# Kernel tuning notes

Hardware: AMD Instinct MI355X
Metric: run time of the kernel (lower is better)

Reference implementation:

```python
import jax, jax.numpy as jnp
import numpy as np

F6_E3M2_MAX = 28.0  # max representable e3m2 value
M_TOKENS, K_IN, N_OUT = 256, 4096, 4096


def _quantize_e3m2(w: np.ndarray) -> np.ndarray:
    """Round-to-nearest onto the FP6 e3m2 grid (bias=3, min normal 2^-2, subnormal step 2^-4)."""
    sign = np.sign(w)
    a = np.minimum(np.abs(w), F6_E3M2_MAX)
    e = np.clip(np.floor(np.log2(np.maximum(a, 1e-30))), -2.0, 4.0)
    step = np.exp2(e - 2.0)  # 2 mantissa bits -> 4 steps per octave; subnormal step = 2^-4
    q = np.round(a / step) * step
    return (sign * np.minimum(q, F6_E3M2_MAX)).astype(np.float32)


def setup_inputs() -> dict:
    key = jax.random.key(0)
    k_x, k_w, k_b = jax.random.split(key, 3)
    x = (jax.random.normal(k_x, (M_TOKENS, K_IN), dtype=jnp.float32)).astype(jnp.float16)
    w_fp32 = np.asarray(jax.random.normal(k_w, (N_OUT, K_IN), dtype=jnp.float32)) * 0.02
    # per-row scale as in to_scaled_tc_float6_e3m2
    amax = np.clip(np.abs(w_fp32).max(axis=1), 1e-12, None)
    scale = F6_E3M2_MAX / amax                       # quantization scale
    weight_fp6 = _quantize_e3m2(w_fp32 * scale[:, None])  # values on the e3m2 grid
    scales = jnp.asarray(1.0 / scale, dtype=jnp.float16)  # dequant scale (stored half)
    bias = (jax.random.normal(k_b, (N_OUT,), dtype=jnp.float32) * 0.01).astype(jnp.float16)
    return {
        "x": x,
        "weight_fp6": jnp.asarray(weight_fp6),
        "scales": scales,
        "bias": bias,
    }


def reference(x, weight_fp6, scales, bias):
    # Fused dequant + GEMM: W = weight_fp6 * row_scale; out = x @ W^T + bias
    in_features = weight_fp6.shape[1]
    x2d = x.reshape(-1, in_features).astype(jnp.float16)
    w_deq = weight_fp6 * scales.astype(jnp.float32)[:, None]  # [N, K] fp32
    out = jnp.einsum("mk,nk->mn", x2d.astype(jnp.float32), w_deq,
                     preferred_element_type=jnp.float32)       # fp32 accumulate (split-K sums in fp32)
    out = out.astype(jnp.float16) + bias
    return out.reshape(*x.shape[:-1], weight_fp6.shape[0]).astype(x.dtype)
```

## Files before the change

kernel.cpp:

```cpp
#include <hip/hip_runtime.h>
#include <hip/hip_fp16.h>


typedef __attribute__((ext_vector_type(8))) _Float16 half8;
typedef __attribute__((ext_vector_type(2))) __fp16 fp16x2;
typedef __attribute__((ext_vector_type(4))) float f32x4;

typedef const __attribute__((address_space(1))) void* gptr_t;
typedef __attribute__((address_space(3))) void* lptr_t;

constexpr int K = 4096, N = 4096, M = 256;
constexpr int BM = 128, BN = 128, BK = 32;
constexpr int SPL = 8;
constexpr int KSPL = K / SPL;
constexpr int NT = KSPL / BK;

__device__ __forceinline__ void gload16(const void* g, void* l) {
    __builtin_amdgcn_global_load_lds((gptr_t)g, (lptr_t)l, 16, 0, 0);
}

__device__ __forceinline__ half8 cvt8(float4 f0, float4 f1) {
    fp16x2 p0 = __builtin_amdgcn_cvt_pkrtz(f0.x, f0.y);
    fp16x2 p1 = __builtin_amdgcn_cvt_pkrtz(f0.z, f0.w);
    fp16x2 p2 = __builtin_amdgcn_cvt_pkrtz(f1.x, f1.y);
    fp16x2 p3 = __builtin_amdgcn_cvt_pkrtz(f1.z, f1.w);
    half8 h;
    h[0]=(_Float16)p0[0]; h[1]=(_Float16)p0[1];
    h[2]=(_Float16)p1[0]; h[3]=(_Float16)p1[1];
    h[4]=(_Float16)p2[0]; h[5]=(_Float16)p2[1];
    h[6]=(_Float16)p3[0]; h[7]=(_Float16)p3[1];
    return h;
}

__global__ __launch_bounds__(256)
void xcvt(const float* __restrict__ X, _Float16* __restrict__ X16)
{
    const int i = ((int)blockIdx.x * 256 + (int)threadIdx.x) * 8;
    float4 a = *(const float4*)(X + i);
    float4 b = *(const float4*)(X + i + 4);
    *(half8*)(X16 + i) = cvt8(a, b);
}

__global__ __launch_bounds__(256, 3)
void gemm(const _Float16* __restrict__ X16,
          const float* __restrict__ W,
          float* __restrict__ P)
{
    __shared__ __align__(16) _Float16 LA[2][BM * BK];
    __shared__ __align__(16) float    LB[2][BN * BK];

    const int tid = (int)threadIdx.x;
    const int l   = tid & 63;
    const int wv  = tid >> 6;
    const int lc  = l & 15;
    const int lr  = l >> 4;
    const int wm  = (wv & 1) * 64;
    const int wn  = (wv >> 1) * 64;

    const int bid = (int)blockIdx.x;
    const int xcd = bid & 7;
    const int i   = bid >> 3;
    const int mb  = i & 1;
    const int sp  = (i >> 1) & 7;
    const int nbl = i >> 4;
    const int bm  = mb * BM;
    const int bn  = (xcd * 4 + nbl) * BN;
    const int kb  = sp * KSPL;

    const int arow = wv * 32 + (l >> 2);
    const int acho = ((l & 3) ^ ((l >> 3) & 3)) * 8;
    const _Float16* ag0 = X16 + (size_t)(bm + arow)      * K + kb + acho;
    const _Float16* ag1 = X16 + (size_t)(bm + arow + 16) * K + kb + acho;
    const int asl0 = (wv * 32) * BK;
    const int asl1 = (wv * 32 + 16) * BK;
    const int wrow = wv * 32 + (l >> 3);
    const int wcho = ((l & 7) ^ (l >> 3)) * 4;
    const float* wg0 = W + (size_t)(bn + wrow)      * K + kb + wcho;
    const float* wg1 = W + (size_t)(bn + wrow + 8)  * K + kb + wcho;
    const float* wg2 = W + (size_t)(bn + wrow + 16) * K + kb + wcho;
    const float* wg3 = W + (size_t)(bn + wrow + 24) * K + kb + wcho;
    const int wsl0 = (wv * 32 + 0)  * BK;
    const int wsl1 = (wv * 32 + 8)  * BK;
    const int wsl2 = (wv * 32 + 16) * BK;
    const int wsl3 = (wv * 32 + 24) * BK;

#define STAGE(t, bf) do {                                               \
        gload16(ag0 + (size_t)(t) * BK, &LA[bf][asl0]);                 \
        gload16(ag1 + (size_t)(t) * BK, &LA[bf][asl1]);                 \
        gload16(wg0 + (size_t)(t) * BK, &LB[bf][wsl0]);                 \
        gload16(wg1 + (size_t)(t) * BK, &LB[bf][wsl1]);                 \
        gload16(wg2 + (size_t)(t) * BK, &LB[bf][wsl2]);                 \
        gload16(wg3 + (size_t)(t) * BK, &LB[bf][wsl3]);                 \
    } while (0)

    const int aswz = (lr ^ ((lc >> 1) & 3)) << 3;
    const int wsz0 = (((lr << 1))     ^ (lc & 7)) << 2;
    const int wsz1 = (((lr << 1) | 1) ^ (lc & 7)) << 2;

    f32x4 acc[4][4];
    #pragma unroll
    for (int a = 0; a < 4; ++a)
        #pragma unroll
        for (int b = 0; b < 4; ++b)
            acc[a][b] = (f32x4){0.f, 0.f, 0.f, 0.f};

#define COMPUTE(bf) do {                                                \
        half8 af[4];                                                    \
        _Pragma("unroll")                                               \
        for (int ar = 0; ar < 4; ++ar)                                  \
            af[ar] = *(const half8*)(&LA[bf][(wm + ar * 16 + lc) * BK + aswz]); \
        _Pragma("unroll")                                               \
        for (int br = 0; br < 4; ++br) {                                \
            const float* pw = &LB[bf][(wn + br * 16 + lc) * BK];        \
            float4 b0 = *(const float4*)(pw + wsz0);                    \
            float4 b1 = *(const float4*)(pw + wsz1);                    \
            half8 bb = cvt8(b0, b1);                                    \
            acc[0][br] = __builtin_amdgcn_mfma_f32_16x16x32_f16(af[0], bb, acc[0][br], 0, 0, 0); \
            acc[1][br] = __builtin_amdgcn_mfma_f32_16x16x32_f16(af[1], bb, acc[1][br], 0, 0, 0); \
            acc[2][br] = __builtin_amdgcn_mfma_f32_16x16x32_f16(af[2], bb, acc[2][br], 0, 0, 0); \
            acc[3][br] = __builtin_amdgcn_mfma_f32_16x16x32_f16(af[3], bb, acc[3][br], 0, 0, 0); \
        } } while (0)

    STAGE(0, 0);

    for (int t = 0; t < NT; ++t) {
        if (t + 1 < NT) {
            STAGE(t + 1, (t + 1) & 1);
            asm volatile("s_waitcnt vmcnt(6)" ::: "memory");
        } else {
            asm volatile("s_waitcnt vmcnt(0)" ::: "memory");
        }
        __builtin_amdgcn_sched_barrier(0);
        __builtin_amdgcn_s_barrier();
        __builtin_amdgcn_sched_barrier(0);
        COMPUTE(t & 1);
        __builtin_amdgcn_sched_barrier(0);
        __builtin_amdgcn_s_barrier();
    }
#undef STAGE
#undef COMPUTE

    float* Pb = P + (size_t)sp * M * N;
    const int orow = bm + wm + lr * 4;
    const int ocol = bn + wn + lc;
    #pragma unroll
    for (int ar = 0; ar < 4; ++ar)
        #pragma unroll
        for (int br = 0; br < 4; ++br)
            #pragma unroll
            for (int r = 0; r < 4; ++r)
                Pb[(size_t)(orow + ar * 16 + r) * N + ocol + br * 16] = acc[ar][br][r];
}

template <int SPLT>
__global__ __launch_bounds__(256)
void finalize(const float* __restrict__ P,
              const float* __restrict__ S,
              const float* __restrict__ Bi,
              float* __restrict__ O)
{
    const size_t i = ((size_t)blockIdx.x * 256 + threadIdx.x) * 4;
    const int n = (int)(i & (N - 1));
    float4 v = *(const float4*)(P + i);
    #pragma unroll
    for (int s = 1; s < SPLT; ++s) {
        float4 u = *(const float4*)(P + (size_t)s * M * N + i);
        v.x += u.x; v.y += u.y; v.z += u.z; v.w += u.w;
    }
    float4 sc = *(const float4*)(S + n);
    float4 bb = *(const float4*)(Bi + n);
    v.x = (float)(_Float16)((float)(_Float16)(v.x * sc.x) + bb.x);
    v.y = (float)(_Float16)((float)(_Float16)(v.y * sc.y) + bb.y);
    v.z = (float)(_Float16)((float)(_Float16)(v.z * sc.z) + bb.z);
    v.w = (float)(_Float16)((float)(_Float16)(v.w * sc.w) + bb.w);
    *(float4*)(O + i) = v;
}

__global__ __launch_bounds__(256)
void fp6lin_small(const float* __restrict__ X, const float* __restrict__ W,
                  const float* __restrict__ S, const float* __restrict__ Bi,
                  float* __restrict__ O)
{
    const int n = (int)blockIdx.x;
    const int m = (int)threadIdx.x;
    float s = 0.f;
    for (int k = 0; k < K; ++k)
        s += (float)(_Float16)X[(size_t)m * K + k] * (float)(_Float16)W[(size_t)n * K + k];
    O[(size_t)m * N + n] = (float)(_Float16)((float)(_Float16)(s * S[n]) + Bi[n]);
}

extern "C" void kernel_launch(void* const* d_in, const int* in_sizes, int n_in,
                              void* d_out, int out_size, void* d_ws, size_t ws_size,
                              hipStream_t stream) {
    const float* x  = (const float*)d_in[0];
    const float* w  = (const float*)d_in[1];
    const float* s  = (const float*)d_in[2];
    const float* bi = (const float*)d_in[3];
    float* o = (float*)d_out;

    const size_t xbytes = (size_t)M * K * 2;
    const size_t slice  = (size_t)M * N * sizeof(float);
    _Float16* x16 = (_Float16*)d_ws;
    float*    P   = (float*)((char*)d_ws + xbytes);
    const int fin_grid = M * N / 4 / 256;

    if (ws_size >= xbytes + SPL * slice) {
        xcvt<<<dim3(M * K / 8 / 256), dim3(256), 0, stream>>>(x, x16);
        gemm<<<dim3(2 * 4 * SPL * 8), dim3(256), 0, stream>>>(x16, w, P);
        finalize<SPL><<<dim3(fin_grid), dim3(256), 0, stream>>>(P, s, bi, o);
    } else {
        fp6lin_small<<<dim3(N), dim3(M), 0, stream>>>(x, w, s, bi, o);
    }
}
```

Measured before the change: 36.75 us.

## Fuse convert, GEMM and split-K reduce into one cooperative kernel

Merges the x fp32-to-fp16 conversion, the split-K GEMM and the finalize reduction into a single cooperative kernel, with grid-wide syncs between the phases. This removes two kernel launches and their inter-kernel gaps. In exchange it adds two grid barriers, and the fused kernel must keep 512 blocks co-resident. If the cooperative launch fails, it falls back to the three separate kernels.

```diff
diff --git a/kernel.cpp b/kernel.cpp
--- a/kernel.cpp
+++ b/kernel.cpp
@@ -1,5 +1,8 @@
 #include <hip/hip_runtime.h>
 #include <hip/hip_fp16.h>
+#include <hip/hip_cooperative_groups.h>
+
+namespace cg = cooperative_groups;
 
 
 typedef __attribute__((ext_vector_type(8))) _Float16 half8;
@@ -32,19 +35,9 @@
     return h;
 }
 
-__global__ __launch_bounds__(256)
-void xcvt(const float* __restrict__ X, _Float16* __restrict__ X16)
-{
-    const int i = ((int)blockIdx.x * 256 + (int)threadIdx.x) * 8;
-    float4 a = *(const float4*)(X + i);
-    float4 b = *(const float4*)(X + i + 4);
-    *(half8*)(X16 + i) = cvt8(a, b);
-}
-
-__global__ __launch_bounds__(256, 3)
-void gemm(const _Float16* __restrict__ X16,
-          const float* __restrict__ W,
-          float* __restrict__ P)
+__device__ __forceinline__ void gemm_body(const _Float16* __restrict__ X16,
+                                          const float* __restrict__ W,
+                                          float* __restrict__ P)
 {
     __shared__ __align__(16) _Float16 LA[2][BM * BK];
     __shared__ __align__(16) float    LB[2][BN * BK];
@@ -122,7 +115,6 @@
         } } while (0)
 
     STAGE(0, 0);
-
     for (int t = 0; t < NT; ++t) {
         if (t + 1 < NT) {
             STAGE(t + 1, (t + 1) & 1);
@@ -152,18 +144,69 @@
                 Pb[(size_t)(orow + ar * 16 + r) * N + ocol + br * 16] = acc[ar][br][r];
 }
 
-template <int SPLT>
+__global__ __launch_bounds__(256, 3)
+void fused(const float* __restrict__ X, const float* __restrict__ W,
+           const float* __restrict__ S, const float* __restrict__ Bi,
+           float* __restrict__ O, _Float16* __restrict__ X16,
+           float* __restrict__ P)
+{
+    {
+        const int i = ((int)blockIdx.x * 256 + (int)threadIdx.x) * 8;
+        float4 a = *(const float4*)(X + i);
+        float4 b = *(const float4*)(X + i + 4);
+        *(half8*)(X16 + i) = cvt8(a, b);
+    }
+    cg::this_grid().sync();
+    gemm_body(X16, W, P);
+    cg::this_grid().sync();
+    {
+        const int gt = (int)blockIdx.x * 256 + (int)threadIdx.x;
+        #pragma unroll
+        for (int rep = 0; rep < 2; ++rep) {
+            const size_t i = ((size_t)(gt * 2 + rep)) * 4;
+            const int n = (int)(i & (N - 1));
+            float4 v = *(const float4*)(P + i);
+            #pragma unroll
+            for (int s = 1; s < SPL; ++s) {
+                float4 u = *(const float4*)(P + (size_t)s * M * N + i);
+                v.x += u.x; v.y += u.y; v.z += u.z; v.w += u.w;
+            }
+            float4 sc = *(const float4*)(S + n);
+            float4 bb = *(const float4*)(Bi + n);
+            v.x = (float)(_Float16)((float)(_Float16)(v.x * sc.x) + bb.x);
+            v.y = (float)(_Float16)((float)(_Float16)(v.y * sc.y) + bb.y);
+            v.z = (float)(_Float16)((float)(_Float16)(v.z * sc.z) + bb.z);
+            v.w = (float)(_Float16)((float)(_Float16)(v.w * sc.w) + bb.w);
+            *(float4*)(O + i) = v;
+        }
+    }
+}
+
 __global__ __launch_bounds__(256)
-void finalize(const float* __restrict__ P,
-              const float* __restrict__ S,
-              const float* __restrict__ Bi,
-              float* __restrict__ O)
+void xcvt(const float* __restrict__ X, _Float16* __restrict__ X16)
+{
+    const int i = ((int)blockIdx.x * 256 + (int)threadIdx.x) * 8;
+    float4 a = *(const float4*)(X + i);
+    float4 b = *(const float4*)(X + i + 4);
+    *(half8*)(X16 + i) = cvt8(a, b);
+}
+
+__global__ __launch_bounds__(256, 3)
+void gemm_k(const _Float16* __restrict__ X16, const float* __restrict__ W,
+            float* __restrict__ P)
+{
+    gemm_body(X16, W, P);
+}
+
+__global__ __launch_bounds__(256)
+void finalize(const float* __restrict__ P, const float* __restrict__ S,
+              const float* __restrict__ Bi, float* __restrict__ O)
 {
     const size_t i = ((size_t)blockIdx.x * 256 + threadIdx.x) * 4;
     const int n = (int)(i & (N - 1));
     float4 v = *(const float4*)(P + i);
     #pragma unroll
-    for (int s = 1; s < SPLT; ++s) {
+    for (int s = 1; s < SPL; ++s) {
         float4 u = *(const float4*)(P + (size_t)s * M * N + i);
         v.x += u.x; v.y += u.y; v.z += u.z; v.w += u.w;
     }
@@ -202,12 +245,18 @@
     const size_t slice  = (size_t)M * N * sizeof(float);
     _Float16* x16 = (_Float16*)d_ws;
     float*    P   = (float*)((char*)d_ws + xbytes);
-    const int fin_grid = M * N / 4 / 256;
 
     if (ws_size >= xbytes + SPL * slice) {
-        xcvt<<<dim3(M * K / 8 / 256), dim3(256), 0, stream>>>(x, x16);
-        gemm<<<dim3(2 * 4 * SPL * 8), dim3(256), 0, stream>>>(x16, w, P);
-        finalize<SPL><<<dim3(fin_grid), dim3(256), 0, stream>>>(P, s, bi, o);
+        void* args[] = { (void*)&x, (void*)&w, (void*)&s, (void*)&bi,
+                         (void*)&o, (void*)&x16, (void*)&P };
+        hipError_t e = hipLaunchCooperativeKernel((const void*)fused,
+                                                  dim3(512), dim3(256),
+                                                  args, 0, stream);
+        if (e != hipSuccess) {
+            xcvt<<<dim3(M * K / 8 / 256), dim3(256), 0, stream>>>(x, x16);
+            gemm_k<<<dim3(512), dim3(256), 0, stream>>>(x16, w, P);
+            finalize<<<dim3(M * N / 4 / 256), dim3(256), 0, stream>>>(P, s, bi, o);
+        }
     } else {
         fp6lin_small<<<dim3(N), dim3(M), 0, stream>>>(x, w, s, bi, o);
     }
```

Result: slower. 146.9 us (+299.8%).

## Fuse x fp16 conversion into GEMM and store split-K partials as fp16

Applied to the files above, without the earlier changes.

Removes the separate xcvt kernel: the GEMM now loads fp32 X tiles straight into LDS and converts to fp16 in registers, the same way it already handles W. Split-K partial sums are written as fp16 instead of fp32, halving partial-buffer traffic, and finalize reads 8 halves per thread. This saves a launch and an X round trip, but doubles the A-tile LDS footprint, which forces occupancy down to 2 blocks per CU. Rounding each partial to fp16 before the fp32 reduction adds error against the reference's fp32 split-K accumulation.

```diff
diff --git a/kernel.cpp b/kernel.cpp
--- a/kernel.cpp
+++ b/kernel.cpp
@@ -32,22 +32,13 @@
     return h;
 }
 
-__global__ __launch_bounds__(256)
-void xcvt(const float* __restrict__ X, _Float16* __restrict__ X16)
+__global__ __launch_bounds__(256, 2)
+void gemm(const float* __restrict__ X,
+          const float* __restrict__ W,
+          _Float16* __restrict__ P)
 {
-    const int i = ((int)blockIdx.x * 256 + (int)threadIdx.x) * 8;
-    float4 a = *(const float4*)(X + i);
-    float4 b = *(const float4*)(X + i + 4);
-    *(half8*)(X16 + i) = cvt8(a, b);
-}
-
-__global__ __launch_bounds__(256, 3)
-void gemm(const _Float16* __restrict__ X16,
-          const float* __restrict__ W,
-          float* __restrict__ P)
-{
-    __shared__ __align__(16) _Float16 LA[2][BM * BK];
-    __shared__ __align__(16) float    LB[2][BN * BK];
+    __shared__ __align__(16) float LA[2][BM * BK];
+    __shared__ __align__(16) float LB[2][BN * BK];
 
     const int tid = (int)threadIdx.x;
     const int l   = tid & 63;
@@ -67,35 +58,34 @@
     const int bn  = (xcd * 4 + nbl) * BN;
     const int kb  = sp * KSPL;
 
-    const int arow = wv * 32 + (l >> 2);
-    const int acho = ((l & 3) ^ ((l >> 3) & 3)) * 8;
-    const _Float16* ag0 = X16 + (size_t)(bm + arow)      * K + kb + acho;
-    const _Float16* ag1 = X16 + (size_t)(bm + arow + 16) * K + kb + acho;
-    const int asl0 = (wv * 32) * BK;
-    const int asl1 = (wv * 32 + 16) * BK;
-    const int wrow = wv * 32 + (l >> 3);
-    const int wcho = ((l & 7) ^ (l >> 3)) * 4;
-    const float* wg0 = W + (size_t)(bn + wrow)      * K + kb + wcho;
-    const float* wg1 = W + (size_t)(bn + wrow + 8)  * K + kb + wcho;
-    const float* wg2 = W + (size_t)(bn + wrow + 16) * K + kb + wcho;
-    const float* wg3 = W + (size_t)(bn + wrow + 24) * K + kb + wcho;
-    const int wsl0 = (wv * 32 + 0)  * BK;
-    const int wsl1 = (wv * 32 + 8)  * BK;
-    const int wsl2 = (wv * 32 + 16) * BK;
-    const int wsl3 = (wv * 32 + 24) * BK;
+    const int srow = wv * 32 + (l >> 3);
+    const int scho = ((l & 7) ^ (l >> 3)) * 4;
+    const float* ag0 = X + (size_t)(bm + srow)      * K + kb + scho;
+    const float* ag1 = X + (size_t)(bm + srow + 8)  * K + kb + scho;
+    const float* ag2 = X + (size_t)(bm + srow + 16) * K + kb + scho;
+    const float* ag3 = X + (size_t)(bm + srow + 24) * K + kb + scho;
+    const float* wg0 = W + (size_t)(bn + srow)      * K + kb + scho;
+    const float* wg1 = W + (size_t)(bn + srow + 8)  * K + kb + scho;
+    const float* wg2 = W + (size_t)(bn + srow + 16) * K + kb + scho;
+    const float* wg3 = W + (size_t)(bn + srow + 24) * K + kb + scho;
+    const int sl0 = (wv * 32 + 0)  * BK;
+    const int sl1 = (wv * 32 + 8)  * BK;
+    const int sl2 = (wv * 32 + 16) * BK;
+    const int sl3 = (wv * 32 + 24) * BK;
 
 #define STAGE(t, bf) do {                                               \
-        gload16(ag0 + (size_t)(t) * BK, &LA[bf][asl0]);                 \
-        gload16(ag1 + (size_t)(t) * BK, &LA[bf][asl1]);                 \
-        gload16(wg0 + (size_t)(t) * BK, &LB[bf][wsl0]);                 \
-        gload16(wg1 + (size_t)(t) * BK, &LB[bf][wsl1]);                 \
-        gload16(wg2 + (size_t)(t) * BK, &LB[bf][wsl2]);                 \
-        gload16(wg3 + (size_t)(t) * BK, &LB[bf][wsl3]);                 \
+        gload16(ag0 + (size_t)(t) * BK, &LA[bf][sl0]);                  \
+        gload16(ag1 + (size_t)(t) * BK, &LA[bf][sl1]);                  \
+        gload16(ag2 + (size_t)(t) * BK, &LA[bf][sl2]);                  \
+        gload16(ag3 + (size_t)(t) * BK, &LA[bf][sl3]);                  \
+        gload16(wg0 + (size_t)(t) * BK, &LB[bf][sl0]);                  \
+        gload16(wg1 + (size_t)(t) * BK, &LB[bf][sl1]);                  \
+        gload16(wg2 + (size_t)(t) * BK, &LB[bf][sl2]);                  \
+        gload16(wg3 + (size_t)(t) * BK, &LB[bf][sl3]);                  \
     } while (0)
 
-    const int aswz = (lr ^ ((lc >> 1) & 3)) << 3;
-    const int wsz0 = (((lr << 1))     ^ (lc & 7)) << 2;
-    const int wsz1 = (((lr << 1) | 1) ^ (lc & 7)) << 2;
+    const int sz0 = (((lr << 1))     ^ (lc & 7)) << 2;
+    const int sz1 = (((lr << 1) | 1) ^ (lc & 7)) << 2;
 
     f32x4 acc[4][4];
     #pragma unroll
@@ -107,14 +97,16 @@
 #define COMPUTE(bf) do {                                                \
         half8 af[4];                                                    \
         _Pragma("unroll")                                               \
-        for (int ar = 0; ar < 4; ++ar)                                  \
-            af[ar] = *(const half8*)(&LA[bf][(wm + ar * 16 + lc) * BK + aswz]); \
+        for (int ar = 0; ar < 4; ++ar) {                                \
+            const float* pa = &LA[bf][(wm + ar * 16 + lc) * BK];        \
+            af[ar] = cvt8(*(const float4*)(pa + sz0),                   \
+                          *(const float4*)(pa + sz1));                  \
+        }                                                               \
         _Pragma("unroll")                                               \
         for (int br = 0; br < 4; ++br) {                                \
             const float* pw = &LB[bf][(wn + br * 16 + lc) * BK];        \
-            float4 b0 = *(const float4*)(pw + wsz0);                    \
-            float4 b1 = *(const float4*)(pw + wsz1);                    \
-            half8 bb = cvt8(b0, b1);                                    \
+            half8 bb = cvt8(*(const float4*)(pw + sz0),                 \
+                            *(const float4*)(pw + sz1));                \
             acc[0][br] = __builtin_amdgcn_mfma_f32_16x16x32_f16(af[0], bb, acc[0][br], 0, 0, 0); \
             acc[1][br] = __builtin_amdgcn_mfma_f32_16x16x32_f16(af[1], bb, acc[1][br], 0, 0, 0); \
             acc[2][br] = __builtin_amdgcn_mfma_f32_16x16x32_f16(af[2], bb, acc[2][br], 0, 0, 0); \
@@ -126,7 +118,7 @@
     for (int t = 0; t < NT; ++t) {
         if (t + 1 < NT) {
             STAGE(t + 1, (t + 1) & 1);
-            asm volatile("s_waitcnt vmcnt(6)" ::: "memory");
+            asm volatile("s_waitcnt vmcnt(8)" ::: "memory");
         } else {
             asm volatile("s_waitcnt vmcnt(0)" ::: "memory");
         }
@@ -140,7 +132,7 @@
 #undef STAGE
 #undef COMPUTE
 
-    float* Pb = P + (size_t)sp * M * N;
+    _Float16* Pb = P + (size_t)sp * M * N;
     const int orow = bm + wm + lr * 4;
     const int ocol = bn + wn + lc;
     #pragma unroll
@@ -149,31 +141,37 @@
         for (int br = 0; br < 4; ++br)
             #pragma unroll
             for (int r = 0; r < 4; ++r)
-                Pb[(size_t)(orow + ar * 16 + r) * N + ocol + br * 16] = acc[ar][br][r];
-}
-
-template <int SPLT>
+                Pb[(size_t)(orow + ar * 16 + r) * N + ocol + br * 16]
+                    = (_Float16)acc[ar][br][r];
+}
+
 __global__ __launch_bounds__(256)
-void finalize(const float* __restrict__ P,
+void finalize(const _Float16* __restrict__ P,
               const float* __restrict__ S,
               const float* __restrict__ Bi,
               float* __restrict__ O)
 {
-    const size_t i = ((size_t)blockIdx.x * 256 + threadIdx.x) * 4;
+    const size_t i = ((size_t)blockIdx.x * 256 + threadIdx.x) * 8;
     const int n = (int)(i & (N - 1));
-    float4 v = *(const float4*)(P + i);
-    #pragma unroll
-    for (int s = 1; s < SPLT; ++s) {
-        float4 u = *(const float4*)(P + (size_t)s * M * N + i);
-        v.x += u.x; v.y += u.y; v.z += u.z; v.w += u.w;
+    float acc[8] = {0.f, 0.f, 0.f, 0.f, 0.f, 0.f, 0.f, 0.f};
+    #pragma unroll
+    for (int s = 0; s < SPL; ++s) {
+        half8 u = *(const half8*)(P + (size_t)s * M * N + i);
+        #pragma unroll
+        for (int e = 0; e < 8; ++e) acc[e] += (float)u[e];
     }
-    float4 sc = *(const float4*)(S + n);
-    float4 bb = *(const float4*)(Bi + n);
-    v.x = (float)(_Float16)((float)(_Float16)(v.x * sc.x) + bb.x);
-    v.y = (float)(_Float16)((float)(_Float16)(v.y * sc.y) + bb.y);
-    v.z = (float)(_Float16)((float)(_Float16)(v.z * sc.z) + bb.z);
-    v.w = (float)(_Float16)((float)(_Float16)(v.w * sc.w) + bb.w);
-    *(float4*)(O + i) = v;
+    float4 sc0 = *(const float4*)(S + n);
+    float4 sc1 = *(const float4*)(S + n + 4);
+    float4 bb0 = *(const float4*)(Bi + n);
+    float4 bb1 = *(const float4*)(Bi + n + 4);
+    float sc[8] = {sc0.x, sc0.y, sc0.z, sc0.w, sc1.x, sc1.y, sc1.z, sc1.w};
+    float bb[8] = {bb0.x, bb0.y, bb0.z, bb0.w, bb1.x, bb1.y, bb1.z, bb1.w};
+    float out[8];
+    #pragma unroll
+    for (int e = 0; e < 8; ++e)
+        out[e] = (float)(_Float16)((float)(_Float16)(acc[e] * sc[e]) + bb[e]);
+    *(float4*)(O + i)     = (float4){out[0], out[1], out[2], out[3]};
+    *(float4*)(O + i + 4) = (float4){out[4], out[5], out[6], out[7]};
 }
 
 __global__ __launch_bounds__(256)
@@ -198,16 +196,12 @@
     const float* bi = (const float*)d_in[3];
     float* o = (float*)d_out;
 
-    const size_t xbytes = (size_t)M * K * 2;
-    const size_t slice  = (size_t)M * N * sizeof(float);
-    _Float16* x16 = (_Float16*)d_ws;
-    float*    P   = (float*)((char*)d_ws + xbytes);
-    const int fin_grid = M * N / 4 / 256;
-
-    if (ws_size >= xbytes + SPL * slice) {
-        xcvt<<<dim3(M * K / 8 / 256), dim3(256), 0, stream>>>(x, x16);
-        gemm<<<dim3(2 * 4 * SPL * 8), dim3(256), 0, stream>>>(x16, w, P);
-        finalize<SPL><<<dim3(fin_grid), dim3(256), 0, stream>>>(P, s, bi, o);
+    const size_t pbytes = (size_t)SPL * M * N * 2;
+    _Float16* P = (_Float16*)d_ws;
+
+    if (ws_size >= pbytes) {
+        gemm<<<dim3(512), dim3(256), 0, stream>>>(x, w, P);
+        finalize<<<dim3(M * N / 8 / 256), dim3(256), 0, stream>>>(P, s, bi, o);
     } else {
         fp6lin_small<<<dim3(N), dim3(M), 0, stream>>>(x, w, s, bi, o);
     }
```

Result: faster. 31.52 us (-14.2%).
